# Kernel tuning notes

Measured on AMD Instinct MI355X. Metric: run time of the kernel, lower is better.

## Reference

```python
import jax, jax.numpy as jnp
import numpy as np

N_WORDS, L, VOCAB, D = 8192, 24, 128, 512
H, DK = 8, 64  # n_head, d_v (=d_k)
N_NAMES, WORDS_PER_NAME = 2048, 4
N_CONCEPTS, NAMES_PER_CONCEPT = 256, 8


def setup_inputs() -> dict:
    key = jax.random.key(0)
    ks = jax.random.split(key, 9)
    s = 1.0 / np.sqrt(D).astype(np.float32)
    inputs = jax.random.randint(ks[0], (N_WORDS, L), 0, VOCAB)  # 0 = pad char
    n_words = jnp.full((N_NAMES,), WORDS_PER_NAME, dtype=jnp.int32)
    n_names = jnp.full((N_CONCEPTS,), NAMES_PER_CONCEPT, dtype=jnp.int32)
    return {
        "inputs": inputs,
        "n_words": n_words,
        "n_names": n_names,
        "emb": jax.random.normal(ks[1], (VOCAB, D), jnp.float32) * s,
        "Wq": jax.random.normal(ks[2], (D, H * DK), jnp.float32) * s,
        "Wk": jax.random.normal(ks[3], (D, H * DK), jnp.float32) * s,
        "Wv": jax.random.normal(ks[4], (D, H * DK), jnp.float32) * s,
        "Wo": jax.random.normal(ks[5], (H * DK, D), jnp.float32) * s,
        "W1": jax.random.normal(ks[6], (D, 512), jnp.float32) * s,
        "W2": jax.random.normal(ks[7], (512, 256), jnp.float32) * s,
    }


def reference(inputs, n_words, n_names, emb, Wq, Wk, Wv, Wo, W1, W2):
    N, Lq = inputs.shape
    pad = inputs == 0  # [N, L] padding mask (char id 0)

    # --- MHAEncoder: embedding + masked multi-head self-attention ---
    x = emb[inputs]  # [N, L, D]
    def split_heads(t):  # [N, L, H*DK] -> [N, H, L, DK]
        return t.reshape(N, Lq, H, DK).transpose(0, 2, 1, 3)
    q = split_heads(x @ Wq)
    k = split_heads(x @ Wk)
    v = split_heads(x @ Wv)
    scale = jnp.asarray(1.0 / np.sqrt(DK), x.dtype)
    scores = jnp.einsum('nhqd,nhkd->nhqk', q, k) * scale  # [N, H, L, L]
    scores = jnp.where(pad[:, None, None, :], jnp.asarray(-1e9, x.dtype), scores)
    attn = jax.nn.softmax(scores, axis=-1)
    o = jnp.einsum('nhqk,nhkd->nhqd', attn, v)
    word_ft = o.transpose(0, 2, 1, 3).reshape(N, Lq, H * DK) @ Wo  # [N, L, D]

    # --- masked mean pooling over chars: matmul(mask, word_ft)/mask.sum(-1) ---
    m = (~pad).astype(word_ft.dtype)  # [N, L]
    name_emb = jnp.einsum('nl,nld->nd', m, word_ft) / m.sum(-1, keepdims=True)  # [N, D]

    # --- split(n_words) + per-group mean == segment mean over word groups ---
    G = n_words.shape[0]
    seg = jnp.repeat(jnp.arange(G), n_words, total_repeat_length=N)
    name_ft = jax.ops.segment_sum(name_emb, seg, num_segments=G)
    name_ft = name_ft / n_words[:, None].astype(name_ft.dtype)  # [G, D]

    # --- small no-bias Tanh MLP ---
    h = jnp.tanh(name_ft @ W1)
    out = jnp.tanh(h @ W2)  # [G, 256]
    # final .split(n_names) is a view-only regrouping; return the packed array
    return out
```

## Files before the change

### kernel.cpp

```cpp
#include <hip/hip_runtime.h>
#include <math.h>

#define NWORDS 8192
#define LW     24
#define VOC    128
#define DIM    512
#define NH     8
#define DKH    64
#define GNAMES 2048
#define F2     256

#define S1_LEN 458752

#define GEMM_BODY(A_, B_, K_, N_, m0_, n0_, kbeg_, kchunk_)                         \
  __shared__ float As[2][16][68];                                                   \
  __shared__ float Bs[2][16][68];                                                   \
  const int t = threadIdx.x, tx = t & 15, ty = t >> 4;                              \
  float acc[4][4] = {};                                                             \
  float ra[4], rb[4];                                                               \
  _Pragma("unroll")                                                                 \
  for (int i = 0; i < 4; ++i) { int idx = t + 256 * i;                              \
    ra[i] = A_[(size_t)(m0_ + (idx >> 4)) * K_ + kbeg_ + (idx & 15)]; }             \
  _Pragma("unroll")                                                                 \
  for (int i = 0; i < 4; ++i) { int idx = t + 256 * i;                              \
    rb[i] = B_[(size_t)(kbeg_ + (idx >> 6)) * N_ + n0_ + (idx & 63)]; }             \
  _Pragma("unroll")                                                                 \
  for (int i = 0; i < 4; ++i) { int idx = t + 256 * i; As[0][idx & 15][idx >> 4] = ra[i]; } \
  _Pragma("unroll")                                                                 \
  for (int i = 0; i < 4; ++i) { int idx = t + 256 * i; Bs[0][idx >> 6][idx & 63] = rb[i]; } \
  __syncthreads();                                                                  \
  int buf = 0;                                                                      \
  for (int k0 = kbeg_; k0 < kbeg_ + kchunk_; k0 += 16) {                            \
    const bool more = (k0 + 16 < kbeg_ + kchunk_);                                  \
    if (more) {                                                                     \
      _Pragma("unroll")                                                             \
      for (int i = 0; i < 4; ++i) { int idx = t + 256 * i;                          \
        ra[i] = A_[(size_t)(m0_ + (idx >> 4)) * K_ + (k0 + 16) + (idx & 15)]; }     \
      _Pragma("unroll")                                                             \
      for (int i = 0; i < 4; ++i) { int idx = t + 256 * i;                          \
        rb[i] = B_[(size_t)(k0 + 16 + (idx >> 6)) * N_ + n0_ + (idx & 63)]; }       \
    }                                                                               \
    _Pragma("unroll")                                                               \
    for (int k = 0; k < 16; ++k) {                                                  \
      float a[4], b[4];                                                             \
      _Pragma("unroll")                                                             \
      for (int i = 0; i < 4; ++i) a[i] = As[buf][k][ty * 4 + i];                    \
      _Pragma("unroll")                                                             \
      for (int j = 0; j < 4; ++j) b[j] = Bs[buf][k][tx * 4 + j];                    \
      _Pragma("unroll")                                                             \
      for (int i = 0; i < 4; ++i)                                                   \
        _Pragma("unroll")                                                           \
        for (int j = 0; j < 4; ++j) acc[i][j] += a[i] * b[j];                       \
    }                                                                               \
    if (more) {                                                                     \
      _Pragma("unroll")                                                             \
      for (int i = 0; i < 4; ++i) { int idx = t + 256 * i; As[buf ^ 1][idx & 15][idx >> 4] = ra[i]; } \
      _Pragma("unroll")                                                             \
      for (int i = 0; i < 4; ++i) { int idx = t + 256 * i; Bs[buf ^ 1][idx >> 6][idx & 63] = rb[i]; } \
      __syncthreads();                                                              \
      buf ^= 1;                                                                     \
    }                                                                               \
  }

template<int NSPLIT>
__global__ __launch_bounds__(256) void k_stage1(const float* __restrict__ emb,
                                                const float* __restrict__ Wq,
                                                const float* __restrict__ Wk,
                                                const float* __restrict__ Wv,
                                                const float* __restrict__ Wo,
                                                const float* __restrict__ W1,
                                                float* __restrict__ P) {
  const int tid = blockIdx.x, s = blockIdx.y;
  const float *A, *B;
  int coff, m0, n0;
  if (tid < 48) {
    const int g = tid >> 4, mt = tid & 15;
    A = emb;
    B = (g == 0) ? Wq : ((g == 1) ? Wk : Wv);
    coff = g * 65536;
    m0 = (mt >> 3) * 64; n0 = (mt & 7) * 64;
  } else {
    const int id = tid - 48;
    A = Wo; B = W1; coff = 3 * 65536;
    m0 = (id >> 3) * 64; n0 = (id & 7) * 64;
  }
  const int kchunk = 512 / NSPLIT, kbeg = s * kchunk;
  GEMM_BODY(A, B, 512, 512, m0, n0, kbeg, kchunk)
  float* Cp = P + (size_t)s * S1_LEN + coff;
  #pragma unroll
  for (int i = 0; i < 4; ++i) {
    float4 v = make_float4(acc[i][0], acc[i][1], acc[i][2], acc[i][3]);
    *(float4*)&Cp[(size_t)(m0 + ty * 4 + i) * 512 + n0 + tx * 4] = v;
  }
}

template<int ACT>
__global__ __launch_bounds__(256) void k_gemm64(const float* __restrict__ A,
                                                const float* __restrict__ B,
                                                float* __restrict__ C,
                                                int M, int N, int K, int kchunk) {
  const int m0 = blockIdx.y * 64, n0 = blockIdx.x * 64;
  const int kbeg = blockIdx.z * kchunk;
  GEMM_BODY(A, B, K, N, m0, n0, kbeg, kchunk)
  float* Cp = C + (size_t)blockIdx.z * M * N;
  #pragma unroll
  for (int i = 0; i < 4; ++i) {
    float4 v = make_float4(acc[i][0], acc[i][1], acc[i][2], acc[i][3]);
    if (ACT) { v.x = tanhf(v.x); v.y = tanhf(v.y); v.z = tanhf(v.z); v.w = tanhf(v.w); }
    *(float4*)&Cp[(size_t)(m0 + ty * 4 + i) * N + n0 + tx * 4] = v;
  }
}

__global__ __launch_bounds__(256) void k_npool(const float* __restrict__ Wn,
                                               const float* __restrict__ EV,
                                               float* __restrict__ NP) {
  const int m0 = blockIdx.x * 64, h = blockIdx.y;
  const float* A2 = Wn + (size_t)m0 * 1024 + h * 128;
  const float* B2 = EV + h * 64;
  GEMM_BODY(A2, B2, 1024, 512, 0, 0, 0, 128)
  #pragma unroll
  for (int i = 0; i < 4; ++i) {
    float4 v = make_float4(acc[i][0], acc[i][1], acc[i][2], acc[i][3]);
    *(float4*)&NP[(size_t)(m0 + ty * 4 + i) * 512 + h * 64 + tx * 4] = v;
  }
}

template<int ACT, int S>
__global__ __launch_bounds__(256) void k_reduce(const float* __restrict__ P,
                                                float* __restrict__ O,
                                                int len4, int stride4) {
  const int i = blockIdx.x * 256 + threadIdx.x;
  if (i >= len4) return;
  const float4* P4 = (const float4*)P;
  float4 a = P4[i];
  #pragma unroll
  for (int s = 1; s < S; ++s) {
    float4 b = P4[(size_t)s * stride4 + i];
    a.x += b.x; a.y += b.y; a.z += b.z; a.w += b.w;
  }
  if (ACT) { a.x = tanhf(a.x); a.y = tanhf(a.y); a.z = tanhf(a.z); a.w = tanhf(a.w); }
  ((float4*)O)[i] = a;
}

__global__ __launch_bounds__(128) void k_qk_tab(const float* __restrict__ EQ,
                                                const float* __restrict__ EK,
                                                float* __restrict__ etab) {
  const int c1 = blockIdx.x, h = blockIdx.y, c2 = threadIdx.x;
  __shared__ float qrow[DKH];
  if (threadIdx.x < DKH) qrow[threadIdx.x] = EQ[c1 * DIM + h * DKH + threadIdx.x];
  __syncthreads();
  const float* krow = EK + c2 * DIM + h * DKH;
  float acc = 0.f;
  #pragma unroll
  for (int d = 0; d < DKH; ++d) acc += qrow[d] * krow[d];
  float e = (c1 != 0 && c2 != 0) ? __expf(acc * 0.125f) : 0.f;
  etab[((size_t)c1 * VOC + c2) * NH + h] = e;
}

__global__ __launch_bounds__(256) void k_scan(const int* __restrict__ nw, int* __restrict__ offs) {
  __shared__ int part[256];
  const int t = threadIdx.x;
  int v[8]; int s = 0;
  #pragma unroll
  for (int i = 0; i < 8; ++i) { v[i] = nw[t * 8 + i]; s += v[i]; }
  part[t] = s;
  __syncthreads();
  if (t == 0) {
    int a = 0;
    for (int i = 0; i < 256; ++i) { int x = part[i]; part[i] = a; a += x; }
    offs[GNAMES] = a;
  }
  __syncthreads();
  int a = part[t];
  #pragma unroll
  for (int i = 0; i < 8; ++i) { offs[t * 8 + i] = a; a += v[i]; }
}

__global__ __launch_bounds__(256) void k_bins(const int* __restrict__ inputs,
                                              const int* __restrict__ offs,
                                              const float* __restrict__ etab,
                                              float* __restrict__ Wn) {
  const int g = blockIdx.x, t = threadIdx.x;
  const int wv = t >> 6, l = t & 63;
  const int h = l & 7, qg = l >> 3;
  const int o0 = offs[g], o1 = offs[g + 1];
  const int nw = o1 - o0;
  __shared__ float bins[VOC * NH];

  for (int i = t; i < VOC * NH; i += 256) bins[i] = 0.f;
  __syncthreads();

  for (int wrel = wv; wrel < nw; wrel += 4) {
    const int wi = o0 + wrel;
    int c_l = (l < LW) ? inputs[(size_t)wi * LW + l] : 0;
    unsigned long long mk = __ballot(c_l != 0);
    int cnt = __popcll(mk);
    float invc = cnt ? 1.f / (float)cnt : 0.f;

    int cq0 = __shfl(c_l, qg);
    int cq1 = __shfl(c_l, qg + 8);
    int cq2 = __shfl(c_l, qg + 16);
    const float* b0 = etab + (cq0 << 10) + h;
    const float* b1 = etab + (cq1 << 10) + h;
    const float* b2 = etab + (cq2 << 10) + h;

    float r0[LW], r1[LW], r2[LW];
    float d0 = 0.f, d1 = 0.f, d2 = 0.f;
    #pragma unroll
    for (int kp = 0; kp < LW; ++kp) {
      int o = __shfl(c_l, kp) << 3;
      r0[kp] = b0[o]; r1[kp] = b1[o]; r2[kp] = b2[o];
      d0 += r0[kp]; d1 += r1[kp]; d2 += r2[kp];
    }
    float i0 = cq0 ? invc / d0 : 0.f;
    float i1 = cq1 ? invc / d1 : 0.f;
    float i2 = cq2 ? invc / d2 : 0.f;

    #pragma unroll
    for (int kp = 0; kp < LW; ++kp) {
      int ck = __shfl(c_l, kp);
      if (ck) {
        float v = r0[kp] * i0 + r1[kp] * i1 + r2[kp] * i2;
        v += __shfl_xor(v, 8);
        v += __shfl_xor(v, 16);
        v += __shfl_xor(v, 32);
        if (qg == 0) atomicAdd(&bins[(ck << 3) + h], v);
      }
    }
  }
  __syncthreads();

  const float invn = nw ? 1.f / (float)nw : 0.f;
  for (int i = t; i < NH * VOC; i += 256) {
    int hh = i >> 7, cc = i & 127;
    Wn[(size_t)g * 1024 + i] = bins[(cc << 3) + hh] * invn;
  }
}

extern "C" void kernel_launch(void* const* d_in, const int* in_sizes, int n_in,
                              void* d_out, int out_size, void* d_ws, size_t ws_size,
                              hipStream_t stream) {
  const int*   inputs  = (const int*)d_in[0];
  const int*   n_words = (const int*)d_in[1];
  const float* emb     = (const float*)d_in[3];
  const float* Wq      = (const float*)d_in[4];
  const float* Wk      = (const float*)d_in[5];
  const float* Wv      = (const float*)d_in[6];
  const float* Wo      = (const float*)d_in[7];
  const float* W1      = (const float*)d_in[8];
  const float* W2      = (const float*)d_in[9];
  float* out = (float*)d_out;

  float* ws  = (float*)d_ws;
  float* ES  = ws;
  float* BIG = ws + 458752;
  float* Wn  = BIG;
  float* TAB = ws + 4653056;
  float* NP  = ws + 4784128;
  float* H1  = ws + 5832704;
  int*  OFFS = (int*)(ws + 6881280);

  k_scan<<<1, 256, 0, stream>>>(n_words, OFFS);
  k_stage1<4><<<dim3(112, 4), 256, 0, stream>>>(emb, Wq, Wk, Wv, Wo, W1, BIG);
  k_reduce<0, 4><<<S1_LEN / 4 / 256, 256, 0, stream>>>(BIG, ES, S1_LEN / 4, S1_LEN / 4);
  k_qk_tab<<<dim3(VOC, NH), 128, 0, stream>>>(ES, ES + 65536, TAB);
  k_bins<<<GNAMES, 256, 0, stream>>>(inputs, OFFS, TAB, Wn);
  k_npool<<<dim3(GNAMES / 64, NH), 256, 0, stream>>>(Wn, ES + 131072, NP);
  k_gemm64<0><<<dim3(8, 32, 4), 256, 0, stream>>>(NP, ES + 196608, BIG, 2048, 512, 512, 128);
  k_reduce<1, 4><<<(GNAMES * DIM) / 4 / 256, 256, 0, stream>>>(BIG, H1, (GNAMES * DIM) / 4, (GNAMES * DIM) / 4);
  k_gemm64<0><<<dim3(4, 32, 4), 256, 0, stream>>>(H1, W2, BIG, 2048, F2, 512, 128);
  k_reduce<1, 4><<<(GNAMES * F2) / 4 / 256, 256, 0, stream>>>(BIG, out, (GNAMES * F2) / 4, (GNAMES * F2) / 4);
}
```

Measured before the change: 108.4 us.

## Fuse scan into bins, bins with name pooling, and split-K reduce into tail GEMM

Removes the separate scan kernel: each bins block now computes its own word offset with a block-wide reduction over n_words. The per-name bin weights are multiplied with the value table inside the same kernel, so the Wn intermediate and the npool GEMM launch go away. The split-K partial sum and tanh that produce H1 are folded into the A-tile load of the second GEMM, which removes another reduce kernel. The cost is redundant work: every block re-reads all of n_words, the tail GEMM recomputes the sum and tanh for each column tile, and the pooling product becomes a scalar per-block loop.

New measurement: 133.2 us. 1.23x slower.

```diff
diff --git a/kernel.cpp b/kernel.cpp
--- a/kernel.cpp
+++ b/kernel.cpp
@@ -11,6 +11,7 @@
 #define F2     256
 
 #define S1_LEN 458752
+#define H1OFF  1048576
 
 #define GEMM_BODY(A_, B_, K_, N_, m0_, n0_, kbeg_, kchunk_)                         \
   __shared__ float As[2][16][68];                                                   \
@@ -111,17 +112,76 @@
   }
 }
 
-__global__ __launch_bounds__(256) void k_npool(const float* __restrict__ Wn,
-                                               const float* __restrict__ EV,
-                                               float* __restrict__ NP) {
-  const int m0 = blockIdx.x * 64, h = blockIdx.y;
-  const float* A2 = Wn + (size_t)m0 * 1024 + h * 128;
-  const float* B2 = EV + h * 64;
-  GEMM_BODY(A2, B2, 1024, 512, 0, 0, 0, 128)
+__global__ __launch_bounds__(256) void k_gemm_tail(const float* __restrict__ P,
+                                                   const float* __restrict__ B,
+                                                   float* __restrict__ C,
+                                                   int kchunk) {
+  const int N = 256, K = 512;
+  __shared__ float As[2][16][68];
+  __shared__ float Bs[2][16][68];
+  const int t = threadIdx.x, tx = t & 15, ty = t >> 4;
+  const int m0 = blockIdx.y * 64, n0 = blockIdx.x * 64;
+  const int kbeg = blockIdx.z * kchunk;
+  float acc[4][4] = {};
+  float ra[4], rb[4];
+  #pragma unroll
+  for (int i = 0; i < 4; ++i) {
+    int idx = t + 256 * i;
+    size_t off = (size_t)(m0 + (idx >> 4)) * K + kbeg + (idx & 15);
+    ra[i] = tanhf(P[off] + P[off + H1OFF] + P[off + 2 * H1OFF] + P[off + 3 * H1OFF]);
+  }
+  #pragma unroll
+  for (int i = 0; i < 4; ++i) {
+    int idx = t + 256 * i;
+    rb[i] = B[(size_t)(kbeg + (idx >> 6)) * N + n0 + (idx & 63)];
+  }
+  #pragma unroll
+  for (int i = 0; i < 4; ++i) { int idx = t + 256 * i; As[0][idx & 15][idx >> 4] = ra[i]; }
+  #pragma unroll
+  for (int i = 0; i < 4; ++i) { int idx = t + 256 * i; Bs[0][idx >> 6][idx & 63] = rb[i]; }
+  __syncthreads();
+  int buf = 0;
+  for (int k0 = kbeg; k0 < kbeg + kchunk; k0 += 16) {
+    const bool more = (k0 + 16 < kbeg + kchunk);
+    if (more) {
+      #pragma unroll
+      for (int i = 0; i < 4; ++i) {
+        int idx = t + 256 * i;
+        size_t off = (size_t)(m0 + (idx >> 4)) * K + (k0 + 16) + (idx & 15);
+        ra[i] = tanhf(P[off] + P[off + H1OFF] + P[off + 2 * H1OFF] + P[off + 3 * H1OFF]);
+      }
+      #pragma unroll
+      for (int i = 0; i < 4; ++i) {
+        int idx = t + 256 * i;
+        rb[i] = B[(size_t)(k0 + 16 + (idx >> 6)) * N + n0 + (idx & 63)];
+      }
+    }
+    #pragma unroll
+    for (int k = 0; k < 16; ++k) {
+      float a[4], b[4];
+      #pragma unroll
+      for (int i = 0; i < 4; ++i) a[i] = As[buf][k][ty * 4 + i];
+      #pragma unroll
+      for (int j = 0; j < 4; ++j) b[j] = Bs[buf][k][tx * 4 + j];
+      #pragma unroll
+      for (int i = 0; i < 4; ++i)
+        #pragma unroll
+        for (int j = 0; j < 4; ++j) acc[i][j] += a[i] * b[j];
+    }
+    if (more) {
+      #pragma unroll
+      for (int i = 0; i < 4; ++i) { int idx = t + 256 * i; As[buf ^ 1][idx & 15][idx >> 4] = ra[i]; }
+      #pragma unroll
+      for (int i = 0; i < 4; ++i) { int idx = t + 256 * i; Bs[buf ^ 1][idx >> 6][idx & 63] = rb[i]; }
+      __syncthreads();
+      buf ^= 1;
+    }
+  }
+  float* Cp = C + (size_t)blockIdx.z * (GNAMES * F2);
   #pragma unroll
   for (int i = 0; i < 4; ++i) {
     float4 v = make_float4(acc[i][0], acc[i][1], acc[i][2], acc[i][3]);
-    *(float4*)&NP[(size_t)(m0 + ty * 4 + i) * 512 + h * 64 + tx * 4] = v;
+    *(float4*)&Cp[(size_t)(m0 + ty * 4 + i) * N + n0 + tx * 4] = v;
   }
 }
 
@@ -157,38 +217,31 @@
   etab[((size_t)c1 * VOC + c2) * NH + h] = e;
 }
 
-__global__ __launch_bounds__(256) void k_scan(const int* __restrict__ nw, int* __restrict__ offs) {
-  __shared__ int part[256];
-  const int t = threadIdx.x;
-  int v[8]; int s = 0;
-  #pragma unroll
-  for (int i = 0; i < 8; ++i) { v[i] = nw[t * 8 + i]; s += v[i]; }
-  part[t] = s;
-  __syncthreads();
-  if (t == 0) {
-    int a = 0;
-    for (int i = 0; i < 256; ++i) { int x = part[i]; part[i] = a; a += x; }
-    offs[GNAMES] = a;
-  }
-  __syncthreads();
-  int a = part[t];
-  #pragma unroll
-  for (int i = 0; i < 8; ++i) { offs[t * 8 + i] = a; a += v[i]; }
-}
-
-__global__ __launch_bounds__(256) void k_bins(const int* __restrict__ inputs,
-                                              const int* __restrict__ offs,
-                                              const float* __restrict__ etab,
-                                              float* __restrict__ Wn) {
+__global__ __launch_bounds__(256) void k_binsnp(const int* __restrict__ inputs,
+                                                const int* __restrict__ nwords,
+                                                const float* __restrict__ etab,
+                                                const float* __restrict__ EV,
+                                                float* __restrict__ NP) {
   const int g = blockIdx.x, t = threadIdx.x;
   const int wv = t >> 6, l = t & 63;
   const int h = l & 7, qg = l >> 3;
-  const int o0 = offs[g], o1 = offs[g + 1];
-  const int nw = o1 - o0;
   __shared__ float bins[VOC * NH];
+  __shared__ int wred[4];
+  __shared__ int sh_nwg;
 
   for (int i = t; i < VOC * NH; i += 256) bins[i] = 0.f;
+  int partial = 0;
+  for (int i = t; i < GNAMES; i += 256) {
+    int v = nwords[i];
+    partial += (i < g) ? v : 0;
+    if (i == g) sh_nwg = v;
+  }
+  #pragma unroll
+  for (int d = 1; d < 64; d <<= 1) partial += __shfl_xor(partial, d);
+  if (l == 0) wred[wv] = partial;
   __syncthreads();
+  const int nw = sh_nwg;
+  const int o0 = wred[0] + wred[1] + wred[2] + wred[3];
 
   for (int wrel = wv; wrel < nw; wrel += 4) {
     const int wi = o0 + wrel;
@@ -231,10 +284,17 @@
   __syncthreads();
 
   const float invn = nw ? 1.f / (float)nw : 0.f;
-  for (int i = t; i < NH * VOC; i += 256) {
-    int hh = i >> 7, cc = i & 127;
-    Wn[(size_t)g * 1024 + i] = bins[(cc << 3) + hh] * invn;
-  }
+  const int h2 = t >> 5;
+  const float2* EV2 = (const float2*)EV;
+  float sx = 0.f, sy = 0.f;
+  #pragma unroll 4
+  for (int c = 0; c < VOC; ++c) {
+    float w = bins[(c << 3) + h2];
+    float2 ev = EV2[c * 256 + t];
+    sx += w * ev.x; sy += w * ev.y;
+  }
+  float2 r; r.x = sx * invn; r.y = sy * invn;
+  ((float2*)NP)[(size_t)g * 256 + t] = r;
 }
 
 extern "C" void kernel_launch(void* const* d_in, const int* in_sizes, int n_in,
@@ -251,23 +311,18 @@
   const float* W2      = (const float*)d_in[9];
   float* out = (float*)d_out;
 
-  float* ws  = (float*)d_ws;
-  float* ES  = ws;
-  float* BIG = ws + 458752;
-  float* Wn  = BIG;
-  float* TAB = ws + 4653056;
-  float* NP  = ws + 4784128;
-  float* H1  = ws + 5832704;
-  int*  OFFS = (int*)(ws + 6881280);
-
-  k_scan<<<1, 256, 0, stream>>>(n_words, OFFS);
+  float* ws   = (float*)d_ws;
+  float* ES   = ws;
+  float* BIG  = ws + 458752;
+  float* TAB  = ws + 4653056;
+  float* NP   = ws + 4784128;
+  float* OUTP = ws + 5832704;
+
   k_stage1<4><<<dim3(112, 4), 256, 0, stream>>>(emb, Wq, Wk, Wv, Wo, W1, BIG);
   k_reduce<0, 4><<<S1_LEN / 4 / 256, 256, 0, stream>>>(BIG, ES, S1_LEN / 4, S1_LEN / 4);
   k_qk_tab<<<dim3(VOC, NH), 128, 0, stream>>>(ES, ES + 65536, TAB);
-  k_bins<<<GNAMES, 256, 0, stream>>>(inputs, OFFS, TAB, Wn);
-  k_npool<<<dim3(GNAMES / 64, NH), 256, 0, stream>>>(Wn, ES + 131072, NP);
+  k_binsnp<<<GNAMES, 256, 0, stream>>>(inputs, n_words, TAB, ES + 131072, NP);
   k_gemm64<0><<<dim3(8, 32, 4), 256, 0, stream>>>(NP, ES + 196608, BIG, 2048, 512, 512, 128);
-  k_reduce<1, 4><<<(GNAMES * DIM) / 4 / 256, 256, 0, stream>>>(BIG, H1, (GNAMES * DIM) / 4, (GNAMES * DIM) / 4);
-  k_gemm64<0><<<dim3(4, 32, 4), 256, 0, stream>>>(H1, W2, BIG, 2048, F2, 512, 128);
-  k_reduce<1, 4><<<(GNAMES * F2) / 4 / 256, 256, 0, stream>>>(BIG, out, (GNAMES * F2) / 4, (GNAMES * F2) / 4);
-}
+  k_gemm_tail<<<dim3(4, 32, 4), 256, 0, stream>>>(BIG, W2, OUTP, 128);
+  k_reduce<1, 4><<<(GNAMES * F2) / 4 / 256, 256, 0, stream>>>(OUTP, out, (GNAMES * F2) / 4, (GNAMES * F2) / 4);
+}
```
